# Kernel optimization log

Measured on AMD Instinct MI355X. Metric: run time of the kernel, lower is better.

## Reference

```python
import jax, jax.numpy as jnp
import numpy as np

N = 100000   # num nodes
E = 3200000  # num edges (avg degree 32)
D = 256      # in_channels
H = 256      # hidden_dim
C = 1        # num_class
G = 512      # num graphs in batch


def setup_inputs() -> dict:
    key = jax.random.key(0)
    k = jax.random.split(key, 5)
    x = jax.random.normal(k[0], (N, D), dtype=jnp.float32)
    edge_index = jax.random.randint(k[1], (2, E), 0, N, dtype=jnp.int64)
    batch = jnp.sort(jax.random.randint(k[2], (N,), 0, G, dtype=jnp.int64))
    # GCNLayer.proj: Linear(D, H); model.lin: Linear(H, C)
    W1 = jax.random.normal(k[3], (H, D), dtype=jnp.float32) * 0.05
    b1 = jnp.zeros((H,), dtype=jnp.float32)
    W2 = jax.random.normal(k[4], (C, H), dtype=jnp.float32) * 0.05
    b2 = jnp.zeros((C,), dtype=jnp.float32)
    return {"x": x, "edge_index": edge_index, "batch": batch,
            "W1": W1, "b1": b1, "W2": W2, "b2": b2}


def reference(x, edge_index, batch, W1, b1, W2, b2):
    src, dst = edge_index[0], edge_index[1]
    # degree(edge_index[0]) over ORIGINAL edges (before self-loops), as in source
    deg = jnp.zeros((N,), x.dtype).at[src].add(jnp.asarray(1.0, x.dtype))
    norm = deg ** -0.5  # D^{-1/2}
    # (D^{-1/2} (A + I) D^{-1/2}) x
    # edge term: out[src] += norm[src] * norm[dst] * x[dst]
    msg = (norm[src] * norm[dst])[:, None] * x[dst]          # [E, D]
    agg = jax.ops.segment_sum(msg, src, num_segments=N)      # [N, D]
    agg = agg + (norm * norm)[:, None] * x                   # self-loop term
    h = jax.nn.relu(agg @ W1.T + b1)                          # [N, H]
    pooled = jax.ops.segment_max(h, batch, num_segments=G)   # [G, H]
    out = pooled @ W2.T + b2                                  # [G, 1]
    return jnp.squeeze(out, axis=1)                           # [G]
```

## Files before the change

kernel.cpp:

```cpp
#include <hip/hip_runtime.h>
#include <cstddef>

#define NN    100000
#define EE    3200000
#define GG    512
#define NBK2  391
#define BCAP  9216
#define TT    4096

typedef __attribute__((ext_vector_type(8))) short bf16x8;
typedef __attribute__((ext_vector_type(4))) float f32x4;
typedef __attribute__((ext_vector_type(8))) unsigned short u16x8;

static __device__ __forceinline__ unsigned short f2b(float f) {
  unsigned u = __float_as_uint(f);
  unsigned r = u + 0x7fffu + ((u >> 16) & 1u);
  return (unsigned short)(r >> 16);
}
static __device__ __forceinline__ float b2f(unsigned short s) {
  return __uint_as_float(((unsigned)s) << 16);
}

__global__ __launch_bounds__(1024, 2) void k_split(const int* __restrict__ src,
                                                   const int* __restrict__ dst,
                                                   int* __restrict__ gcur,
                                                   int* __restrict__ pk) {
  __shared__ int hist[NBK2], st[NBK2], cur[NBK2], gbase[NBK2];
  __shared__ int sc[512];
  __shared__ int sorted[TT];
  __shared__ unsigned short binof[TT];
  const int tid  = threadIdx.x;
  const int e_lo = blockIdx.x * (EE / 256);
  const int e_hi = e_lo + (EE / 256);

  for (int t0 = e_lo; t0 < e_hi; t0 += TT) {
    const int tc = min(TT, e_hi - t0);
    if (tid < NBK2) hist[tid] = 0;
    __syncthreads();
    int myk[4], myw[4];
#pragma unroll
    for (int r = 0; r < 4; ++r) {
      int j = r * 1024 + tid;
      myk[r] = -1;
      if (j < tc) {
        int s = src[t0 + j], d = dst[t0 + j];
        myk[r] = s >> 8;
        myw[r] = ((s & 255) << 17) | d;
        atomicAdd(&hist[myk[r]], 1);
      }
    }
    __syncthreads();
    if (tid < 512) sc[tid] = (tid < NBK2) ? hist[tid] : 0;
    __syncthreads();
    for (int d = 1; d < 512; d <<= 1) {
      int v = (tid < 512 && tid >= d) ? sc[tid - d] : 0;
      __syncthreads();
      if (tid < 512) sc[tid] += v;
      __syncthreads();
    }
    if (tid < NBK2) { st[tid] = tid ? sc[tid - 1] : 0; cur[tid] = st[tid]; }
    __syncthreads();
#pragma unroll
    for (int r = 0; r < 4; ++r) {
      if (myk[r] >= 0) {
        int pos = atomicAdd(&cur[myk[r]], 1);
        sorted[pos] = myw[r];
        binof[pos] = (unsigned short)myk[r];
      }
    }
    __syncthreads();
    if (tid < NBK2) {
      int c = cur[tid] - st[tid];
      gbase[tid] = c ? atomicAdd(&gcur[tid], c) : 0;
    }
    __syncthreads();
    for (int j = tid; j < tc; j += 1024) {
      int k   = binof[j];
      int idx = gbase[k] + (j - st[k]);
      if (idx < BCAP) pk[(size_t)k * BCAP + idx] = sorted[j];
    }
    __syncthreads();
  }
}

__global__ __launch_bounds__(512) void k_prep(const int* __restrict__ gcur,
                                              const int* __restrict__ pk,
                                              const float* __restrict__ x,
                                              const float* __restrict__ w1,
                                              unsigned short* __restrict__ ybf,
                                              unsigned short* __restrict__ wbf,
                                              int* __restrict__ csr,
                                              int* __restrict__ ro) {
  __shared__ int hist[256], start[257], cur[256], sc[256];
  const int tid = threadIdx.x;
  const int b   = blockIdx.x;
  const int n0  = b * 256;

  if (tid < 256) hist[tid] = 0;
  __syncthreads();
  const int szc = min(gcur[b], BCAP);
  const int* __restrict__ pb = pk + (size_t)b * BCAP;
  for (int j = tid; j < szc; j += 512)
    atomicAdd(&hist[pb[j] >> 17], 1);
  __syncthreads();
  if (tid < 256) sc[tid] = hist[tid];
  __syncthreads();
  for (int d = 1; d < 256; d <<= 1) {
    int v = (tid < 256 && tid >= d) ? sc[tid - d] : 0;
    __syncthreads();
    if (tid < 256) sc[tid] += v;
    __syncthreads();
  }
  if (tid < 256) { start[tid] = tid ? sc[tid - 1] : 0; cur[tid] = start[tid]; }
  if (tid == 0) start[256] = 0;
  __syncthreads();
  if (tid == 0) start[256] = sc[255];
  __syncthreads();
  for (int j = tid; j < szc; j += 512) {
    int w = pb[j];
    int pos = atomicAdd(&cur[w >> 17], 1);
    csr[(size_t)b * BCAP + pos] = w & 0x1FFFF;
  }
  if (tid < 257) ro[b * 257 + tid] = start[tid];

  for (int it = 0; it < 32; ++it) {
    int idx = it * 512 + tid;
    int row = idx >> 6, c4 = idx & 63;
    int n = n0 + row;
    if (n < NN) {
      float nr = rsqrtf((float)(start[row + 1] - start[row]));
      float4 v = ((const float4*)x)[(size_t)n * 64 + c4];
      ushort4 o;
      o.x = f2b(nr * v.x); o.y = f2b(nr * v.y); o.z = f2b(nr * v.z); o.w = f2b(nr * v.w);
      ((ushort4*)ybf)[(size_t)n * 64 + c4] = o;
    }
  }
  if (b < 64 && tid < 256) {
    int i = b * 256 + tid;
    float4 v = ((const float4*)w1)[i];
    ushort4 o;
    o.x = f2b(v.x); o.y = f2b(v.y); o.z = f2b(v.z); o.w = f2b(v.w);
    ((ushort4*)wbf)[i] = o;
  }
}

__global__ __launch_bounds__(512, 8) void k_fused4(const int* __restrict__ ro,
                                                   const int* __restrict__ csr,
                                                   const unsigned short* __restrict__ ybf,
                                                   const unsigned short* __restrict__ wbf,
                                                   const float* __restrict__ b1,
                                                   const int* __restrict__ batch,
                                                   int* __restrict__ pooled) {
  __shared__ __align__(16) unsigned short As[16][264];
  __shared__ int rs[17];
  __shared__ int bg[16];
  const int tid  = threadIdx.x;
  const int n0   = blockIdx.x * 16;
  const int bkt  = blockIdx.x >> 4;
  const int br   = (blockIdx.x & 15) * 16;
  const int wave = tid >> 6;
  const int lane = tid & 63;

  if (tid < 17) rs[tid] = ro[bkt * 257 + br + tid];
  else if (tid >= 64 && tid < 80) bg[tid - 64] = batch[n0 + tid - 64];
  __syncthreads();

  const int half = lane >> 5, l32 = lane & 31;
  const int il   = wave * 2 + half;
  const int i    = n0 + il;
  const u16x8* __restrict__ yr = (const u16x8*)ybf;
  const int* __restrict__ ce = csr + (size_t)bkt * BCAP;

  u16x8 sv = yr[(size_t)i * 32 + l32];
  float acc[8];
#pragma unroll
  for (int c = 0; c < 8; ++c) acc[c] = b2f(sv[c]);

  int e = rs[il];
  const int e1 = rs[il + 1];
  const float ni = rsqrtf((float)(e1 - e));
  for (; e + 8 <= e1; e += 8) {
    int d0 = ce[e],     d1 = ce[e + 1], d2 = ce[e + 2], d3 = ce[e + 3];
    int d4 = ce[e + 4], d5 = ce[e + 5], d6 = ce[e + 6], d7 = ce[e + 7];
    u16x8 v0 = yr[(size_t)d0 * 32 + l32];
    u16x8 v1 = yr[(size_t)d1 * 32 + l32];
    u16x8 v2 = yr[(size_t)d2 * 32 + l32];
    u16x8 v3 = yr[(size_t)d3 * 32 + l32];
    u16x8 v4 = yr[(size_t)d4 * 32 + l32];
    u16x8 v5 = yr[(size_t)d5 * 32 + l32];
    u16x8 v6 = yr[(size_t)d6 * 32 + l32];
    u16x8 v7 = yr[(size_t)d7 * 32 + l32];
#pragma unroll
    for (int c = 0; c < 8; ++c)
      acc[c] += ((b2f(v0[c]) + b2f(v1[c])) + (b2f(v2[c]) + b2f(v3[c]))) +
                ((b2f(v4[c]) + b2f(v5[c])) + (b2f(v6[c]) + b2f(v7[c])));
  }
  for (; e + 4 <= e1; e += 4) {
    int d0 = ce[e], d1 = ce[e + 1], d2 = ce[e + 2], d3 = ce[e + 3];
    u16x8 v0 = yr[(size_t)d0 * 32 + l32];
    u16x8 v1 = yr[(size_t)d1 * 32 + l32];
    u16x8 v2 = yr[(size_t)d2 * 32 + l32];
    u16x8 v3 = yr[(size_t)d3 * 32 + l32];
#pragma unroll
    for (int c = 0; c < 8; ++c)
      acc[c] += (b2f(v0[c]) + b2f(v1[c])) + (b2f(v2[c]) + b2f(v3[c]));
  }
  for (; e < e1; ++e) {
    u16x8 v = yr[(size_t)ce[e] * 32 + l32];
#pragma unroll
    for (int c = 0; c < 8; ++c) acc[c] += b2f(v[c]);
  }
  u16x8 o;
#pragma unroll
  for (int c = 0; c < 8; ++c) o[c] = f2b(ni * acc[c]);
  *(u16x8*)&As[il][l32 * 8] = o;
  __syncthreads();

  const int r16 = lane & 15, quad = lane >> 4;
  f32x4 acc4[2];
#pragma unroll
  for (int t = 0; t < 2; ++t) acc4[t] = (f32x4){0.f, 0.f, 0.f, 0.f};
  for (int kc = 0; kc < 8; ++kc) {
    bf16x8 af = *(const bf16x8*)&As[r16][kc * 32 + quad * 8];
#pragma unroll
    for (int ct = 0; ct < 2; ++ct) {
      const int n = wave * 32 + ct * 16 + r16;
      bf16x8 bf = *(const bf16x8*)(wbf + (size_t)n * 256 + kc * 32 + quad * 8);
      acc4[ct] = __builtin_amdgcn_mfma_f32_16x16x32_bf16(af, bf, acc4[ct], 0, 0, 0);
    }
  }

  const int g0 = bg[0], g15 = bg[15];
  if (g0 == g15) {
#pragma unroll
    for (int ct = 0; ct < 2; ++ct) {
      const int col = wave * 32 + ct * 16 + r16;
      const float bias = b1[col];
      float m = 0.f;
#pragma unroll
      for (int r = 0; r < 4; ++r) m = fmaxf(m, acc4[ct][r] + bias);
      m = fmaxf(m, __shfl_xor(m, 16, 64));
      m = fmaxf(m, __shfl_xor(m, 32, 64));
      if (quad == 0) atomicMax(&pooled[g0 * 256 + col], __float_as_int(m));
    }
  } else {
#pragma unroll
    for (int ct = 0; ct < 2; ++ct) {
      const int col = wave * 32 + ct * 16 + r16;
      const float bias = b1[col];
      for (int g = g0; g <= g15; ++g) {
        float m = 0.f;
#pragma unroll
        for (int r = 0; r < 4; ++r) {
          const int row = quad * 4 + r;
          float v = fmaxf(acc4[ct][r] + bias, 0.f);
          if (bg[row] == g) m = fmaxf(m, v);
        }
        m = fmaxf(m, __shfl_xor(m, 16, 64));
        m = fmaxf(m, __shfl_xor(m, 32, 64));
        if (quad == 0) atomicMax(&pooled[g * 256 + col], __float_as_int(m));
      }
    }
  }
}

__global__ void k_out(const float* __restrict__ pooled, const float* __restrict__ w2,
                      const float* __restrict__ b2, float* __restrict__ out) {
  const int wave = threadIdx.x >> 6;
  const int lane = threadIdx.x & 63;
  const int g = blockIdx.x * 4 + wave;
  float4 p = ((const float4*)pooled)[g * 64 + lane];
  float4 w = ((const float4*)w2)[lane];
  float s = p.x * w.x + p.y * w.y + p.z * w.z + p.w * w.w;
  for (int off = 32; off; off >>= 1) s += __shfl_down(s, off, 64);
  if (lane == 0) out[g] = s + b2[0];
}

extern "C" void kernel_launch(void* const* d_in, const int* in_sizes, int n_in,
                              void* d_out, int out_size, void* d_ws, size_t ws_size,
                              hipStream_t stream) {
  const float* x     = (const float*)d_in[0];
  const int*   ei    = (const int*)d_in[1];
  const int*   batch = (const int*)d_in[2];
  const float* W1    = (const float*)d_in[3];
  const float* b1    = (const float*)d_in[4];
  const float* W2    = (const float*)d_in[5];
  const float* b2    = (const float*)d_in[6];
  const int* src = ei;
  const int* dst = ei + EE;
  float* out = (float*)d_out;

  size_t off = 0;
  auto carve = [&](size_t bytes) -> void* {
    void* p = (char*)d_ws + off;
    off += (bytes + 255) & ~(size_t)255;
    return p;
  };
  int*   pooled = (int*)carve((size_t)GG * 256 * 4);
  int*   gcur   = (int*)carve((size_t)NBK2 * 4);
  const size_t zlen = off;
  unsigned short* ybf = (unsigned short*)carve((size_t)NN * 256 * 2);
  int*   pk     = (int*)carve((size_t)NBK2 * BCAP * 4);
  int*   csr    = (int*)carve((size_t)NBK2 * BCAP * 4);
  int*   ro     = (int*)carve((size_t)NBK2 * 257 * 4);
  unsigned short* wbf = (unsigned short*)carve(256 * 256 * 2);

  hipMemsetAsync(pooled, 0, zlen, stream);

  k_split<<<256,     1024, 0, stream>>>(src, dst, gcur, pk);
  k_prep <<<NBK2,     512, 0, stream>>>(gcur, pk, x, W1, ybf, wbf, csr, ro);
  k_fused4<<<NN / 16, 512, 0, stream>>>(ro, csr, ybf, wbf, b1, batch, pooled);
  k_out  <<<GG / 4,   256, 0, stream>>>((const float*)pooled, W2, b2, out);
}
```

Measured before the change: 465.8 us.

## Quantize gathered features to 12-bit packed ints with global max scale

Replaces the bf16 normalized feature table with a 12-bit fixed-point encoding: k_prep computes a global max of norm-scaled |x| and a new k_pack kernel quantizes and packs 8 values into 12 bytes. The gather-aggregate loop then sums integers and dequantizes once per row, shrinking the random-gather traffic from 16 to 12 bytes per lane. It also flattens k_split to one tile per block with more blocks. The cost is an extra kernel pass over x, an extra read of x, and reduced precision (12-bit uniform quantization against a global max) that may exceed tolerance.

```diff
diff --git a/kernel.cpp b/kernel.cpp
--- a/kernel.cpp
+++ b/kernel.cpp
@@ -12,13 +12,12 @@
 typedef __attribute__((ext_vector_type(4))) float f32x4;
 typedef __attribute__((ext_vector_type(8))) unsigned short u16x8;
 
+struct U12 { unsigned a, b, c; };
+
 static __device__ __forceinline__ unsigned short f2b(float f) {
   unsigned u = __float_as_uint(f);
   unsigned r = u + 0x7fffu + ((u >> 16) & 1u);
   return (unsigned short)(r >> 16);
-}
-static __device__ __forceinline__ float b2f(unsigned short s) {
-  return __uint_as_float(((unsigned)s) << 16);
 }
 
 __global__ __launch_bounds__(1024, 2) void k_split(const int* __restrict__ src,
@@ -29,57 +28,53 @@
   __shared__ int sc[512];
   __shared__ int sorted[TT];
   __shared__ unsigned short binof[TT];
-  const int tid  = threadIdx.x;
-  const int e_lo = blockIdx.x * (EE / 256);
-  const int e_hi = e_lo + (EE / 256);
-
-  for (int t0 = e_lo; t0 < e_hi; t0 += TT) {
-    const int tc = min(TT, e_hi - t0);
-    if (tid < NBK2) hist[tid] = 0;
+  const int tid = threadIdx.x;
+  const int t0  = blockIdx.x * TT;
+  const int tc  = min(TT, EE - t0);
+
+  if (tid < NBK2) hist[tid] = 0;
+  __syncthreads();
+  int myk[4], myw[4];
+#pragma unroll
+  for (int r = 0; r < 4; ++r) {
+    int j = r * 1024 + tid;
+    myk[r] = -1;
+    if (j < tc) {
+      int s = src[t0 + j], d = dst[t0 + j];
+      myk[r] = s >> 8;
+      myw[r] = ((s & 255) << 17) | d;
+      atomicAdd(&hist[myk[r]], 1);
+    }
+  }
+  __syncthreads();
+  if (tid < 512) sc[tid] = (tid < NBK2) ? hist[tid] : 0;
+  __syncthreads();
+  for (int d = 1; d < 512; d <<= 1) {
+    int v = (tid < 512 && tid >= d) ? sc[tid - d] : 0;
     __syncthreads();
-    int myk[4], myw[4];
-#pragma unroll
-    for (int r = 0; r < 4; ++r) {
-      int j = r * 1024 + tid;
-      myk[r] = -1;
-      if (j < tc) {
-        int s = src[t0 + j], d = dst[t0 + j];
-        myk[r] = s >> 8;
-        myw[r] = ((s & 255) << 17) | d;
-        atomicAdd(&hist[myk[r]], 1);
-      }
-    }
+    if (tid < 512) sc[tid] += v;
     __syncthreads();
-    if (tid < 512) sc[tid] = (tid < NBK2) ? hist[tid] : 0;
-    __syncthreads();
-    for (int d = 1; d < 512; d <<= 1) {
-      int v = (tid < 512 && tid >= d) ? sc[tid - d] : 0;
-      __syncthreads();
-      if (tid < 512) sc[tid] += v;
-      __syncthreads();
-    }
-    if (tid < NBK2) { st[tid] = tid ? sc[tid - 1] : 0; cur[tid] = st[tid]; }
-    __syncthreads();
-#pragma unroll
-    for (int r = 0; r < 4; ++r) {
-      if (myk[r] >= 0) {
-        int pos = atomicAdd(&cur[myk[r]], 1);
-        sorted[pos] = myw[r];
-        binof[pos] = (unsigned short)myk[r];
-      }
-    }
-    __syncthreads();
-    if (tid < NBK2) {
-      int c = cur[tid] - st[tid];
-      gbase[tid] = c ? atomicAdd(&gcur[tid], c) : 0;
-    }
-    __syncthreads();
-    for (int j = tid; j < tc; j += 1024) {
-      int k   = binof[j];
-      int idx = gbase[k] + (j - st[k]);
-      if (idx < BCAP) pk[(size_t)k * BCAP + idx] = sorted[j];
-    }
-    __syncthreads();
+  }
+  if (tid < NBK2) { st[tid] = tid ? sc[tid - 1] : 0; cur[tid] = st[tid]; }
+  __syncthreads();
+#pragma unroll
+  for (int r = 0; r < 4; ++r) {
+    if (myk[r] >= 0) {
+      int pos = atomicAdd(&cur[myk[r]], 1);
+      sorted[pos] = myw[r];
+      binof[pos] = (unsigned short)myk[r];
+    }
+  }
+  __syncthreads();
+  if (tid < NBK2) {
+    int c = cur[tid] - st[tid];
+    gbase[tid] = c ? atomicAdd(&gcur[tid], c) : 0;
+  }
+  __syncthreads();
+  for (int j = tid; j < tc; j += 1024) {
+    int k   = binof[j];
+    int idx = gbase[k] + (j - st[k]);
+    if (idx < BCAP) pk[(size_t)k * BCAP + idx] = sorted[j];
   }
 }
 
@@ -87,11 +82,12 @@
                                               const int* __restrict__ pk,
                                               const float* __restrict__ x,
                                               const float* __restrict__ w1,
-                                              unsigned short* __restrict__ ybf,
                                               unsigned short* __restrict__ wbf,
                                               int* __restrict__ csr,
-                                              int* __restrict__ ro) {
+                                              int* __restrict__ ro,
+                                              int* __restrict__ xm) {
   __shared__ int hist[256], start[257], cur[256], sc[256];
+  __shared__ float red[8];
   const int tid = threadIdx.x;
   const int b   = blockIdx.x;
   const int n0  = b * 256;
@@ -112,7 +108,6 @@
     __syncthreads();
   }
   if (tid < 256) { start[tid] = tid ? sc[tid - 1] : 0; cur[tid] = start[tid]; }
-  if (tid == 0) start[256] = 0;
   __syncthreads();
   if (tid == 0) start[256] = sc[255];
   __syncthreads();
@@ -122,19 +117,32 @@
     csr[(size_t)b * BCAP + pos] = w & 0x1FFFF;
   }
   if (tid < 257) ro[b * 257 + tid] = start[tid];
-
+  __syncthreads();
+
+  float tmax = 0.f;
   for (int it = 0; it < 32; ++it) {
     int idx = it * 512 + tid;
     int row = idx >> 6, c4 = idx & 63;
     int n = n0 + row;
-    if (n < NN) {
-      float nr = rsqrtf((float)(start[row + 1] - start[row]));
+    int deg = start[row + 1] - start[row];
+    if (n < NN && deg > 0) {
+      float nr = rsqrtf((float)deg);
       float4 v = ((const float4*)x)[(size_t)n * 64 + c4];
-      ushort4 o;
-      o.x = f2b(nr * v.x); o.y = f2b(nr * v.y); o.z = f2b(nr * v.z); o.w = f2b(nr * v.w);
-      ((ushort4*)ybf)[(size_t)n * 64 + c4] = o;
-    }
-  }
+      float m = fmaxf(fmaxf(fabsf(v.x), fabsf(v.y)), fmaxf(fabsf(v.z), fabsf(v.w)));
+      tmax = fmaxf(tmax, nr * m);
+    }
+  }
+#pragma unroll
+  for (int k = 1; k < 64; k <<= 1) tmax = fmaxf(tmax, __shfl_xor(tmax, k, 64));
+  if ((tid & 63) == 0) red[tid >> 6] = tmax;
+  __syncthreads();
+  if (tid == 0) {
+    float m = red[0];
+#pragma unroll
+    for (int w = 1; w < 8; ++w) m = fmaxf(m, red[w]);
+    atomicMax(xm, __float_as_int(m));
+  }
+
   if (b < 64 && tid < 256) {
     int i = b * 256 + tid;
     float4 v = ((const float4*)w1)[i];
@@ -144,12 +152,43 @@
   }
 }
 
+__global__ __launch_bounds__(256) void k_pack(const float* __restrict__ x,
+                                              const int* __restrict__ ro,
+                                              const int* __restrict__ xm,
+                                              unsigned* __restrict__ y12) {
+  const int tid = threadIdx.x;
+  const int row = blockIdx.x * 8 + (tid >> 5);
+  const int l32 = tid & 31;
+  const int bkt = row >> 8, r = row & 255;
+  const int deg = ro[bkt * 257 + r + 1] - ro[bkt * 257 + r];
+  const float nr  = rsqrtf((float)deg);
+  const float s   = __int_as_float(*xm);
+  const float inv = 2047.0f / s;
+
+  float4 a = ((const float4*)x)[(size_t)row * 64 + l32 * 2];
+  float4 b = ((const float4*)x)[(size_t)row * 64 + l32 * 2 + 1];
+  int q[8];
+  float v[8] = {a.x, a.y, a.z, a.w, b.x, b.y, b.z, b.w};
+#pragma unroll
+  for (int c = 0; c < 8; ++c) {
+    int t = (int)rintf(nr * v[c] * inv) + 2048;
+    q[c] = min(4095, max(0, t));
+  }
+  U12 o;
+  o.a = (unsigned)q[0] | ((unsigned)q[1] << 12) | ((unsigned)(q[2] & 0xFF) << 24);
+  o.b = ((unsigned)q[2] >> 8) | ((unsigned)q[3] << 4) | ((unsigned)q[4] << 16) |
+        ((unsigned)(q[5] & 0xF) << 28);
+  o.c = ((unsigned)q[5] >> 4) | ((unsigned)q[6] << 8) | ((unsigned)q[7] << 20);
+  ((U12*)y12)[(size_t)row * 32 + l32] = o;
+}
+
 __global__ __launch_bounds__(512, 8) void k_fused4(const int* __restrict__ ro,
                                                    const int* __restrict__ csr,
-                                                   const unsigned short* __restrict__ ybf,
+                                                   const unsigned* __restrict__ y12,
                                                    const unsigned short* __restrict__ wbf,
                                                    const float* __restrict__ b1,
                                                    const int* __restrict__ batch,
+                                                   const int* __restrict__ xm,
                                                    int* __restrict__ pooled) {
   __shared__ __align__(16) unsigned short As[16][264];
   __shared__ int rs[17];
@@ -168,51 +207,61 @@
   const int half = lane >> 5, l32 = lane & 31;
   const int il   = wave * 2 + half;
   const int i    = n0 + il;
-  const u16x8* __restrict__ yr = (const u16x8*)ybf;
+  const U12* __restrict__ yr = (const U12*)y12;
   const int* __restrict__ ce = csr + (size_t)bkt * BCAP;
-
-  u16x8 sv = yr[(size_t)i * 32 + l32];
-  float acc[8];
-#pragma unroll
-  for (int c = 0; c < 8; ++c) acc[c] = b2f(sv[c]);
+  const float s = __int_as_float(*xm);
+
+  int acc[8];
+#pragma unroll
+  for (int c = 0; c < 8; ++c) acc[c] = 0;
+#define UNP(V) do { unsigned w0 = (V).a, w1 = (V).b, w2 = (V).c;                  \
+    acc[0] += (int)(w0 & 0xFFFu);                                                 \
+    acc[1] += (int)((w0 >> 12) & 0xFFFu);                                         \
+    acc[2] += (int)((w0 >> 24) | ((w1 & 0xFu) << 8));                             \
+    acc[3] += (int)((w1 >> 4) & 0xFFFu);                                          \
+    acc[4] += (int)((w1 >> 16) & 0xFFFu);                                         \
+    acc[5] += (int)((w1 >> 28) | ((w2 & 0xFFu) << 4));                            \
+    acc[6] += (int)((w2 >> 8) & 0xFFFu);                                          \
+    acc[7] += (int)(w2 >> 20); } while (0)
+
+  U12 sv = yr[(size_t)i * 32 + l32];
+  UNP(sv);
 
   int e = rs[il];
   const int e1 = rs[il + 1];
+  const int cnt = e1 - e + 1;
   const float ni = rsqrtf((float)(e1 - e));
   for (; e + 8 <= e1; e += 8) {
     int d0 = ce[e],     d1 = ce[e + 1], d2 = ce[e + 2], d3 = ce[e + 3];
     int d4 = ce[e + 4], d5 = ce[e + 5], d6 = ce[e + 6], d7 = ce[e + 7];
-    u16x8 v0 = yr[(size_t)d0 * 32 + l32];
-    u16x8 v1 = yr[(size_t)d1 * 32 + l32];
-    u16x8 v2 = yr[(size_t)d2 * 32 + l32];
-    u16x8 v3 = yr[(size_t)d3 * 32 + l32];
-    u16x8 v4 = yr[(size_t)d4 * 32 + l32];
-    u16x8 v5 = yr[(size_t)d5 * 32 + l32];
-    u16x8 v6 = yr[(size_t)d6 * 32 + l32];
-    u16x8 v7 = yr[(size_t)d7 * 32 + l32];
-#pragma unroll
-    for (int c = 0; c < 8; ++c)
-      acc[c] += ((b2f(v0[c]) + b2f(v1[c])) + (b2f(v2[c]) + b2f(v3[c]))) +
-                ((b2f(v4[c]) + b2f(v5[c])) + (b2f(v6[c]) + b2f(v7[c])));
+    U12 v0 = yr[(size_t)d0 * 32 + l32];
+    U12 v1 = yr[(size_t)d1 * 32 + l32];
+    U12 v2 = yr[(size_t)d2 * 32 + l32];
+    U12 v3 = yr[(size_t)d3 * 32 + l32];
+    U12 v4 = yr[(size_t)d4 * 32 + l32];
+    U12 v5 = yr[(size_t)d5 * 32 + l32];
+    U12 v6 = yr[(size_t)d6 * 32 + l32];
+    U12 v7 = yr[(size_t)d7 * 32 + l32];
+    UNP(v0); UNP(v1); UNP(v2); UNP(v3); UNP(v4); UNP(v5); UNP(v6); UNP(v7);
   }
   for (; e + 4 <= e1; e += 4) {
     int d0 = ce[e], d1 = ce[e + 1], d2 = ce[e + 2], d3 = ce[e + 3];
-    u16x8 v0 = yr[(size_t)d0 * 32 + l32];
-    u16x8 v1 = yr[(size_t)d1 * 32 + l32];
-    u16x8 v2 = yr[(size_t)d2 * 32 + l32];
-    u16x8 v3 = yr[(size_t)d3 * 32 + l32];
-#pragma unroll
-    for (int c = 0; c < 8; ++c)
-      acc[c] += (b2f(v0[c]) + b2f(v1[c])) + (b2f(v2[c]) + b2f(v3[c]));
+    U12 v0 = yr[(size_t)d0 * 32 + l32];
+    U12 v1 = yr[(size_t)d1 * 32 + l32];
+    U12 v2 = yr[(size_t)d2 * 32 + l32];
+    U12 v3 = yr[(size_t)d3 * 32 + l32];
+    UNP(v0); UNP(v1); UNP(v2); UNP(v3);
   }
   for (; e < e1; ++e) {
-    u16x8 v = yr[(size_t)ce[e] * 32 + l32];
-#pragma unroll
-    for (int c = 0; c < 8; ++c) acc[c] += b2f(v[c]);
-  }
+    U12 v = yr[(size_t)ce[e] * 32 + l32];
+    UNP(v);
+  }
+#undef UNP
+  const float fsc = ni * s * (1.0f / 2047.0f);
+  const float boff = 2048.0f * (float)cnt;
   u16x8 o;
 #pragma unroll
-  for (int c = 0; c < 8; ++c) o[c] = f2b(ni * acc[c]);
+  for (int c = 0; c < 8; ++c) o[c] = f2b(fsc * ((float)acc[c] - boff));
   *(u16x8*)&As[il][l32 * 8] = o;
   __syncthreads();
 
@@ -298,8 +347,9 @@
   };
   int*   pooled = (int*)carve((size_t)GG * 256 * 4);
   int*   gcur   = (int*)carve((size_t)NBK2 * 4);
+  int*   xm     = (int*)carve(4);
   const size_t zlen = off;
-  unsigned short* ybf = (unsigned short*)carve((size_t)NN * 256 * 2);
+  unsigned* y12 = (unsigned*)carve((size_t)NN * 96 * 4);
   int*   pk     = (int*)carve((size_t)NBK2 * BCAP * 4);
   int*   csr    = (int*)carve((size_t)NBK2 * BCAP * 4);
   int*   ro     = (int*)carve((size_t)NBK2 * 257 * 4);
@@ -307,8 +357,9 @@
 
   hipMemsetAsync(pooled, 0, zlen, stream);
 
-  k_split<<<256,     1024, 0, stream>>>(src, dst, gcur, pk);
-  k_prep <<<NBK2,     512, 0, stream>>>(gcur, pk, x, W1, ybf, wbf, csr, ro);
-  k_fused4<<<NN / 16, 512, 0, stream>>>(ro, csr, ybf, wbf, b1, batch, pooled);
-  k_out  <<<GG / 4,   256, 0, stream>>>((const float*)pooled, W2, b2, out);
-}
+  k_split<<<(EE + TT - 1) / TT, 1024, 0, stream>>>(src, dst, gcur, pk);
+  k_prep <<<NBK2,               512,  0, stream>>>(gcur, pk, x, W1, wbf, csr, ro, xm);
+  k_pack <<<NN / 8,             256,  0, stream>>>(x, ro, xm, y12);
+  k_fused4<<<NN / 16,           512,  0, stream>>>(ro, csr, y12, wbf, b1, batch, xm, pooled);
+  k_out  <<<GG / 4,             256,  0, stream>>>((const float*)pooled, W2, b2, out);
+}
```

Result: faster. 441.9 us (-5.1%).
